# Kernel optimization log

Measured on AMD Instinct MI355X. Metric: run time of the kernel, lower is better.

## Reference

```python
import jax, jax.numpy as jnp
import numpy as np

# WeightOnlyInt8Linear forward: out = (x @ W_int8.astype(x.dtype).T) * scales
# NOTE: the original torch forward has a bug: when bias is not None it returns
# pre_bias (bias is never added), and when bias is None it would crash.
# Faithful math for a runnable configuration (bias=True) is therefore just
# the scaled matmul without bias.

IN_FEATURES = 4096
OUT_FEATURES = 16384
M = 256  # tokens


def setup_inputs() -> dict:
    key = jax.random.key(0)
    k1, k2, k3 = jax.random.split(key, 3)
    x = jax.random.normal(k1, (M, IN_FEATURES), dtype=jnp.float32)
    # int8 quantized weights in [-128, 127]
    weight = jax.random.randint(k2, (OUT_FEATURES, IN_FEATURES), -128, 128, dtype=jnp.int8)
    # per-output-channel dequant scales (positive, small)
    scales = jax.random.uniform(k3, (OUT_FEATURES,), dtype=jnp.float32, minval=0.001, maxval=0.02)
    return {"input": x, "weight": weight, "scales": scales}


def reference(input, weight, scales):
    # weight.to(input): upcast int8 -> activation dtype, then dense GEMM, then per-channel scale
    w = weight.astype(input.dtype)                      # [out, in]
    pre_bias = jnp.einsum('mk,nk->mn', input, w)        # [M, out]
    return pre_bias * scales                            # broadcast over out_features
```

## Files before the change

### kernel.cpp

```cpp
#include <hip/hip_runtime.h>
#include <stdint.h>

#define M_TOK 256
#define N_OUT 16384
#define K_IN  4096
#define BM 64
#define BN 128
#define BK 64
#define NSTEPS (K_IN / BK)

#define AS1 __attribute__((address_space(1)))
#define AS3 __attribute__((address_space(3)))

typedef short v8s __attribute__((ext_vector_type(8)));
typedef float v16f __attribute__((ext_vector_type(16)));
typedef int   v4i __attribute__((ext_vector_type(4)));
typedef unsigned int uint;

__device__ __forceinline__ unsigned short rne_bf16(float f) {
  uint u = __float_as_uint(f);
  uint r = u + 0x7FFFu + ((u >> 16) & 1u);
  return (unsigned short)(r >> 16);
}
__device__ __forceinline__ float bfbits_to_f(uint h) {
  return __uint_as_float(h << 16);
}
__device__ __forceinline__ uint pack_bf16(float a, float b) {
  return (__float_as_uint(a) >> 16) | (__float_as_uint(b) & 0xffff0000u);
}

__global__ __launch_bounds__(256) void cast_kernel(
    const float* __restrict__ x, unsigned short* __restrict__ xhi,
    unsigned short* __restrict__ xlo) {
  const int i = (blockIdx.x * 256 + threadIdx.x) * 4;
  const float4 f = *(const float4*)(x + i);
  float fs[4] = {f.x, f.y, f.z, f.w};
  unsigned short h[4], l[4];
#pragma unroll
  for (int j = 0; j < 4; ++j) {
    h[j] = rne_bf16(fs[j]);
    l[j] = rne_bf16(fs[j] - bfbits_to_f(h[j]));
  }
  *(ushort4*)(xhi + i) = make_ushort4(h[0], h[1], h[2], h[3]);
  *(ushort4*)(xlo + i) = make_ushort4(l[0], l[1], l[2], l[3]);
}

__global__ __launch_bounds__(256, 2) void gemm_kernel(
    const unsigned short* __restrict__ xhi, const unsigned short* __restrict__ xlo,
    const void* __restrict__ wraw, const float* __restrict__ scales,
    float* __restrict__ out) {
  __shared__ alignas(16) unsigned char smem[65536];
  const int tid = threadIdx.x;
  const int lane = tid & 63;
  const int wid = tid >> 6;

  const int* wi = (const int*)wraw;
  const signed char* wb = (const signed char*)wraw;
  bool is32 = true;
#pragma unroll
  for (int i = 0; i < 16; ++i) {
    const int v = wi[i];
    is32 = is32 && (v >= -128) && (v <= 127);
  }

  const int bid = blockIdx.x;
  const int logical = (bid & 7) * 64 + (bid >> 3);
  const int mb = logical & 3;
  const int nb = logical >> 2;
  const int m0 = mb * BM;
  const int n0 = nb * BN;

  const unsigned short* xsrc[4];
  uint xdst[4];
#pragma unroll
  for (int j = 0; j < 4; ++j) {
    const int s = wid * 4 + j;
    const int r = 4 * s + (lane >> 4);
    const int c = (lane & 15) ^ (r & 15);
    xsrc[j] = xhi + (size_t)(c >> 3) * M_TOK * K_IN
            + (size_t)(m0 + r) * K_IN + (size_t)((c & 7) * 8);
    xdst[j] = (uint)(s * 1024);
  }

  const int wr32 = tid >> 4, wc32 = tid & 15;
  const int* w32base = wi + (size_t)(n0 + wr32) * K_IN + (size_t)(wc32 * 4);
  const int wr8 = tid >> 2, wc8 = tid & 3;
  const signed char* w8base = wb + (size_t)(n0 + wr8) * K_IN + (size_t)(wc8 * 16);

  const int l31 = lane & 31, hi5 = lane >> 5;
  const int wm = (wid & 1) * 32;
  const int wn = (wid >> 1) * 64;
  const uint abase = (uint)((wm + l31) * 256);
  const uint axor = (uint)((wm + l31) & 15);
  uint bbase[2], bxor[2], bsel[2];
#pragma unroll
  for (int nf = 0; nf < 2; ++nf) {
    const int wrow = wn + nf * 32 + l31;
    const int q = wrow >> 1;
    bbase[nf] = (uint)(q * 256);
    bxor[nf] = (uint)(q & 15);
    bsel[nf] = (uint)((wrow & 1) * 8);
  }

  v16f acc[2] = {};
  v4i wt[8];

  auto stage = [&](int s, uint xb) {
#pragma unroll
    for (int j = 0; j < 4; ++j)
      __builtin_amdgcn_global_load_lds(
          (const AS1 void*)(xsrc[j] + (size_t)s * BK),
          (AS3 void*)(smem + xb + xdst[j]), 16, 0, 0);
    if (is32) {
#pragma unroll
      for (int i = 0; i < 8; ++i)
        wt[i] = *(const v4i*)(w32base + (size_t)i * 16 * K_IN + (size_t)s * 64);
    } else {
#pragma unroll
      for (int i = 0; i < 2; ++i)
        wt[i] = *(const v4i*)(w8base + (size_t)i * 64 * K_IN + (size_t)s * 64);
    }
  };

  auto conv_write_w = [&](uint wo) {
    if (is32) {
#pragma unroll
      for (int i = 0; i < 8; ++i) {
        const int r = i * 16 + wr32;
        const int q = r >> 1;
        const int chunk = (r & 1) * 8 + (wc32 >> 1);
        const uint byte = wo + (uint)(q * 256) + (uint)((chunk ^ (q & 15)) << 4) +
                          (uint)((wc32 & 1) * 8);
        uint2 d;
        d.x = pack_bf16((float)wt[i].x, (float)wt[i].y);
        d.y = pack_bf16((float)wt[i].z, (float)wt[i].w);
        *(uint2*)(smem + byte) = d;
      }
    } else {
#pragma unroll
      for (int i = 0; i < 2; ++i) {
        const int r = i * 64 + wr8;
        const int q = r >> 1;
        const signed char* bs = (const signed char*)&wt[i];
        uint u[4];
#pragma unroll
        for (int p = 0; p < 4; ++p)
          u[p] = pack_bf16((float)bs[2 * p], (float)bs[2 * p + 1]);
        uint u2[4];
#pragma unroll
        for (int p = 0; p < 4; ++p)
          u2[p] = pack_bf16((float)bs[8 + 2 * p], (float)bs[8 + 2 * p + 1]);
        const int cb = (r & 1) * 8 + wc8 * 2;
        const uint b0 = wo + (uint)(q * 256) + (uint)(((cb + 0) ^ (q & 15)) << 4);
        const uint b1 = wo + (uint)(q * 256) + (uint)(((cb + 1) ^ (q & 15)) << 4);
        *(v4i*)(smem + b0) = *(v4i*)&u[0];
        *(v4i*)(smem + b1) = *(v4i*)&u2[0];
      }
    }
  };

  stage(0, 0u);
  conv_write_w(32768u);
  __syncthreads();

  for (int t = 0; t < NSTEPS; ++t) {
    const uint cur = (uint)(t & 1) << 14;
    const uint xb = cur, wo = 32768u + cur;
    const uint nxb = xb ^ 16384u, nwo = wo ^ 16384u;
    const bool more = (t + 1 < NSTEPS);
    if (more) stage(t + 1, nxb);
    __builtin_amdgcn_sched_barrier(0);

#pragma unroll
    for (int kc = 0; kc < 4; ++kc) {
      const uint ch = (uint)(kc * 2 + hi5);
      v8s ah = *(const v8s*)(smem + xb + abase + ((ch ^ axor) << 4));
      v8s al = *(const v8s*)(smem + xb + abase + (((ch + 8u) ^ axor) << 4));
      v8s b0 = *(const v8s*)(smem + wo + bbase[0] + (((bsel[0] + ch) ^ bxor[0]) << 4));
      v8s b1 = *(const v8s*)(smem + wo + bbase[1] + (((bsel[1] + ch) ^ bxor[1]) << 4));
      acc[0] = __builtin_amdgcn_mfma_f32_32x32x16_bf16(ah, b0, acc[0], 0, 0, 0);
      acc[0] = __builtin_amdgcn_mfma_f32_32x32x16_bf16(al, b0, acc[0], 0, 0, 0);
      acc[1] = __builtin_amdgcn_mfma_f32_32x32x16_bf16(ah, b1, acc[1], 0, 0, 0);
      acc[1] = __builtin_amdgcn_mfma_f32_32x32x16_bf16(al, b1, acc[1], 0, 0, 0);
    }

    if (more) conv_write_w(nwo);
    __syncthreads();
  }

#pragma unroll
  for (int nf = 0; nf < 2; ++nf) {
    const int n = n0 + wn + nf * 32 + l31;
    const float scl = scales[n];
#pragma unroll
    for (int reg = 0; reg < 16; ++reg) {
      const int m = m0 + wm + (reg & 3) + 8 * (reg >> 2) + 4 * hi5;
      out[(size_t)m * N_OUT + n] = acc[nf][reg] * scl;
    }
  }
}

__global__ void naive_kernel(const float* __restrict__ x, const void* __restrict__ wraw,
                             const float* __restrict__ scales, float* __restrict__ out) {
  const int* wi = (const int*)wraw;
  bool is32 = true;
  for (int i = 0; i < 16; ++i) { int v = wi[i]; is32 = is32 && v >= -128 && v <= 127; }
  const int idx = blockIdx.x * 256 + threadIdx.x;
  const int m = idx >> 14;
  const int n = idx & (N_OUT - 1);
  const float* xr = x + (size_t)m * K_IN;
  float acc = 0.f;
  if (is32) {
    const int* wr = wi + (size_t)n * K_IN;
    for (int k = 0; k < K_IN; ++k) acc += xr[k] * (float)wr[k];
  } else {
    const signed char* wr = (const signed char*)wraw + (size_t)n * K_IN;
    for (int k = 0; k < K_IN; ++k) acc += xr[k] * (float)wr[k];
  }
  out[idx] = acc * scales[n];
}

extern "C" void kernel_launch(void* const* d_in, const int* in_sizes, int n_in,
                              void* d_out, int out_size, void* d_ws, size_t ws_size,
                              hipStream_t stream) {
  const float* x = (const float*)d_in[0];
  const void* w = d_in[1];
  const float* scales = (const float*)d_in[2];
  float* out = (float*)d_out;
  if (ws_size >= (size_t)4 * 1024 * 1024) {
    unsigned short* xhi = (unsigned short*)d_ws;
    unsigned short* xlo = xhi + (size_t)M_TOK * K_IN;
    cast_kernel<<<(M_TOK * K_IN) / 1024, 256, 0, stream>>>(x, xhi, xlo);
    gemm_kernel<<<512, 256, 0, stream>>>(xhi, xlo, w, scales, out);
  } else {
    naive_kernel<<<(M_TOK * N_OUT) / 256, 256, 0, stream>>>(x, w, scales, out);
  }
}
```

Measured before the change: 496.2 us.

## Double BK, single-buffer LDS, and prefetch weights two steps ahead in registers

Raises the K tile from 64 to 128, which halves the number of loop iterations and barriers. Shared memory becomes a single buffer: x hi and lo planes go to separate 16KB regions and weights use a plain row-major swizzle. Weight global loads are issued two steps ahead into registers, while the x tile for the next step is loaded asynchronously into LDS between two barriers, with hand-written vmcnt/lgkmcnt waits. The aim is to hide global weight latency behind MFMA work. The cost is double the weight registers, which may hurt occupancy, plus two barriers per step and exposed x-load latency because LDS is no longer double-buffered.

```diff
diff --git a/kernel.cpp b/kernel.cpp
--- a/kernel.cpp
+++ b/kernel.cpp
@@ -6,7 +6,7 @@
 #define K_IN  4096
 #define BM 64
 #define BN 128
-#define BK 64
+#define BK 128
 #define NSTEPS (K_IN / BK)
 
 #define AS1 __attribute__((address_space(1)))
@@ -70,122 +70,127 @@
   const int m0 = mb * BM;
   const int n0 = nb * BN;
 
-  const unsigned short* xsrc[4];
-  uint xdst[4];
-#pragma unroll
-  for (int j = 0; j < 4; ++j) {
-    const int s = wid * 4 + j;
-    const int r = 4 * s + (lane >> 4);
-    const int c = (lane & 15) ^ (r & 15);
-    xsrc[j] = xhi + (size_t)(c >> 3) * M_TOK * K_IN
-            + (size_t)(m0 + r) * K_IN + (size_t)((c & 7) * 8);
-    xdst[j] = (uint)(s * 1024);
-  }
-
-  const int wr32 = tid >> 4, wc32 = tid & 15;
-  const int* w32base = wi + (size_t)(n0 + wr32) * K_IN + (size_t)(wc32 * 4);
-  const int wr8 = tid >> 2, wc8 = tid & 3;
-  const signed char* w8base = wb + (size_t)(n0 + wr8) * K_IN + (size_t)(wc8 * 16);
+  const unsigned short* xsrc[8];
+  uint xdst[8];
+#pragma unroll
+  for (int j = 0; j < 8; ++j) {
+    const int s = wid * 8 + j;
+    const int plane = s >> 4;
+    const int sp = s & 15;
+    const int r = sp * 4 + (lane >> 4);
+    const int p = (lane & 15) ^ (r & 15);
+    xsrc[j] = (plane ? xlo : xhi) + (size_t)(m0 + r) * K_IN + (size_t)(p * 8);
+    xdst[j] = (uint)(plane * 16384 + sp * 1024);
+  }
+
+  const int trow = tid >> 5, c32 = tid & 31;
+  const int* w32base = wi + (size_t)(n0 + trow) * K_IN + (size_t)(c32 * 4);
+  const int r8 = tid >> 3, c8 = tid & 7;
+  const signed char* w8base = wb + (size_t)(n0 + r8) * K_IN + (size_t)(c8 * 16);
 
   const int l31 = lane & 31, hi5 = lane >> 5;
   const int wm = (wid & 1) * 32;
   const int wn = (wid >> 1) * 64;
-  const uint abase = (uint)((wm + l31) * 256);
+  const uint arow = (uint)((wm + l31) * 256);
   const uint axor = (uint)((wm + l31) & 15);
-  uint bbase[2], bxor[2], bsel[2];
+  uint brow[2], bxor[2];
 #pragma unroll
   for (int nf = 0; nf < 2; ++nf) {
-    const int wrow = wn + nf * 32 + l31;
-    const int q = wrow >> 1;
-    bbase[nf] = (uint)(q * 256);
-    bxor[nf] = (uint)(q & 15);
-    bsel[nf] = (uint)((wrow & 1) * 8);
+    const int wr = wn + nf * 32 + l31;
+    brow[nf] = 32768u + (uint)(wr * 256);
+    bxor[nf] = (uint)(wr & 15);
   }
 
   v16f acc[2] = {};
-  v4i wt[8];
-
-  auto stage = [&](int s, uint xb) {
-#pragma unroll
-    for (int j = 0; j < 4; ++j)
+  v4i wt[16];
+
+  auto stage_x = [&](int s) {
+#pragma unroll
+    for (int j = 0; j < 8; ++j)
       __builtin_amdgcn_global_load_lds(
           (const AS1 void*)(xsrc[j] + (size_t)s * BK),
-          (AS3 void*)(smem + xb + xdst[j]), 16, 0, 0);
+          (AS3 void*)(smem + xdst[j]), 16, 0, 0);
+  };
+  auto load_w = [&](int s) {
     if (is32) {
 #pragma unroll
-      for (int i = 0; i < 8; ++i)
-        wt[i] = *(const v4i*)(w32base + (size_t)i * 16 * K_IN + (size_t)s * 64);
+      for (int i = 0; i < 16; ++i)
+        wt[i] = *(const v4i*)(w32base + (size_t)i * 8 * K_IN + (size_t)s * BK);
     } else {
 #pragma unroll
-      for (int i = 0; i < 2; ++i)
-        wt[i] = *(const v4i*)(w8base + (size_t)i * 64 * K_IN + (size_t)s * 64);
+      for (int i = 0; i < 4; ++i)
+        wt[i] = *(const v4i*)(w8base + (size_t)i * 32 * K_IN + (size_t)s * BK);
     }
   };
-
-  auto conv_write_w = [&](uint wo) {
+  auto conv_w = [&]() {
     if (is32) {
 #pragma unroll
-      for (int i = 0; i < 8; ++i) {
-        const int r = i * 16 + wr32;
-        const int q = r >> 1;
-        const int chunk = (r & 1) * 8 + (wc32 >> 1);
-        const uint byte = wo + (uint)(q * 256) + (uint)((chunk ^ (q & 15)) << 4) +
-                          (uint)((wc32 & 1) * 8);
+      for (int i = 0; i < 16; ++i) {
+        const int row = i * 8 + trow;
+        const uint a = 32768u + (uint)(row * 256) +
+                       (uint)(((c32 >> 1) ^ (row & 15)) << 4) + (uint)((c32 & 1) * 8);
         uint2 d;
         d.x = pack_bf16((float)wt[i].x, (float)wt[i].y);
         d.y = pack_bf16((float)wt[i].z, (float)wt[i].w);
-        *(uint2*)(smem + byte) = d;
+        *(uint2*)(smem + a) = d;
       }
     } else {
 #pragma unroll
-      for (int i = 0; i < 2; ++i) {
-        const int r = i * 64 + wr8;
-        const int q = r >> 1;
+      for (int i = 0; i < 4; ++i) {
+        const int row = i * 32 + r8;
         const signed char* bs = (const signed char*)&wt[i];
-        uint u[4];
-#pragma unroll
-        for (int p = 0; p < 4; ++p)
-          u[p] = pack_bf16((float)bs[2 * p], (float)bs[2 * p + 1]);
-        uint u2[4];
-#pragma unroll
-        for (int p = 0; p < 4; ++p)
-          u2[p] = pack_bf16((float)bs[8 + 2 * p], (float)bs[8 + 2 * p + 1]);
-        const int cb = (r & 1) * 8 + wc8 * 2;
-        const uint b0 = wo + (uint)(q * 256) + (uint)(((cb + 0) ^ (q & 15)) << 4);
-        const uint b1 = wo + (uint)(q * 256) + (uint)(((cb + 1) ^ (q & 15)) << 4);
-        *(v4i*)(smem + b0) = *(v4i*)&u[0];
-        *(v4i*)(smem + b1) = *(v4i*)&u2[0];
+        uint u0[4], u1[4];
+#pragma unroll
+        for (int p = 0; p < 4; ++p) {
+          u0[p] = pack_bf16((float)bs[2 * p], (float)bs[2 * p + 1]);
+          u1[p] = pack_bf16((float)bs[8 + 2 * p], (float)bs[8 + 2 * p + 1]);
+        }
+        const uint base = 32768u + (uint)(row * 256);
+        const uint a0 = base + (uint)(((2 * c8 + 0) ^ (row & 15)) << 4);
+        const uint a1 = base + (uint)(((2 * c8 + 1) ^ (row & 15)) << 4);
+        *(v4i*)(smem + a0) = *(v4i*)&u0[0];
+        *(v4i*)(smem + a1) = *(v4i*)&u1[0];
       }
     }
   };
 
-  stage(0, 0u);
-  conv_write_w(32768u);
-  __syncthreads();
-
-  for (int t = 0; t < NSTEPS; ++t) {
-    const uint cur = (uint)(t & 1) << 14;
-    const uint xb = cur, wo = 32768u + cur;
-    const uint nxb = xb ^ 16384u, nwo = wo ^ 16384u;
-    const bool more = (t + 1 < NSTEPS);
-    if (more) stage(t + 1, nxb);
-    __builtin_amdgcn_sched_barrier(0);
-
-#pragma unroll
-    for (int kc = 0; kc < 4; ++kc) {
+  stage_x(0);
+  load_w(0);
+  conv_w();
+  load_w(1);
+  asm volatile("s_waitcnt lgkmcnt(0)" ::: "memory");
+  __builtin_amdgcn_s_barrier();
+  __builtin_amdgcn_sched_barrier(0);
+
+  for (int t = 0;; ++t) {
+#pragma unroll
+    for (int kc = 0; kc < 8; ++kc) {
       const uint ch = (uint)(kc * 2 + hi5);
-      v8s ah = *(const v8s*)(smem + xb + abase + ((ch ^ axor) << 4));
-      v8s al = *(const v8s*)(smem + xb + abase + (((ch + 8u) ^ axor) << 4));
-      v8s b0 = *(const v8s*)(smem + wo + bbase[0] + (((bsel[0] + ch) ^ bxor[0]) << 4));
-      v8s b1 = *(const v8s*)(smem + wo + bbase[1] + (((bsel[1] + ch) ^ bxor[1]) << 4));
+      v8s ah = *(const v8s*)(smem + arow + ((ch ^ axor) << 4));
+      v8s al = *(const v8s*)(smem + 16384u + arow + ((ch ^ axor) << 4));
+      v8s b0 = *(const v8s*)(smem + brow[0] + ((ch ^ bxor[0]) << 4));
+      v8s b1 = *(const v8s*)(smem + brow[1] + ((ch ^ bxor[1]) << 4));
       acc[0] = __builtin_amdgcn_mfma_f32_32x32x16_bf16(ah, b0, acc[0], 0, 0, 0);
       acc[0] = __builtin_amdgcn_mfma_f32_32x32x16_bf16(al, b0, acc[0], 0, 0, 0);
       acc[1] = __builtin_amdgcn_mfma_f32_32x32x16_bf16(ah, b1, acc[1], 0, 0, 0);
       acc[1] = __builtin_amdgcn_mfma_f32_32x32x16_bf16(al, b1, acc[1], 0, 0, 0);
     }
-
-    if (more) conv_write_w(nwo);
-    __syncthreads();
+    if (t == NSTEPS - 1) break;
+
+    asm volatile("s_waitcnt lgkmcnt(0)" ::: "memory");
+    __builtin_amdgcn_s_barrier();
+    __builtin_amdgcn_sched_barrier(0);
+
+    stage_x(t + 1);
+    conv_w();
+    asm volatile("" ::: "memory");
+    const int wnext = (t + 2 < NSTEPS) ? t + 2 : NSTEPS - 1;
+    load_w(wnext);
+    if (is32) asm volatile("s_waitcnt vmcnt(16)" ::: "memory");
+    else      asm volatile("s_waitcnt vmcnt(4)" ::: "memory");
+    asm volatile("s_waitcnt lgkmcnt(0)" ::: "memory");
+    __builtin_amdgcn_s_barrier();
+    __builtin_amdgcn_sched_barrier(0);
   }
 
 #pragma unroll
```

After: 471.0 us. 5.1% less time.

## Reshape GEMM tile to 128x64 with 512 threads and single-buffered LDS

Applied to the files above, without the earlier changes.

Changes the block tile from 64x128 to 128x64, so each weight row is read by two M-blocks instead of four. This roughly halves global weight traffic, which dominates when the weights arrive as int32. The block now has 8 waves, each computing one 32x32 fragment, and uses a single LDS buffer with smaller shared memory to allow more resident blocks. The trade-offs are doubled activation re-reads and the loss of double-buffered overlap between loading and MFMA compute.

```diff
diff --git a/kernel.cpp b/kernel.cpp
--- a/kernel.cpp
+++ b/kernel.cpp
@@ -4,8 +4,8 @@
 #define M_TOK 256
 #define N_OUT 16384
 #define K_IN  4096
-#define BM 64
-#define BN 128
+#define BM 128
+#define BN 64
 #define BK 64
 #define NSTEPS (K_IN / BK)
 
@@ -45,11 +45,11 @@
   *(ushort4*)(xlo + i) = make_ushort4(l[0], l[1], l[2], l[3]);
 }
 
-__global__ __launch_bounds__(256, 2) void gemm_kernel(
+__global__ __launch_bounds__(512, 4) void gemm_kernel(
     const unsigned short* __restrict__ xhi, const unsigned short* __restrict__ xlo,
     const void* __restrict__ wraw, const float* __restrict__ scales,
     float* __restrict__ out) {
-  __shared__ alignas(16) unsigned char smem[65536];
+  __shared__ alignas(16) unsigned char smem[40960];
   const int tid = threadIdx.x;
   const int lane = tid & 63;
   const int wid = tid >> 6;
@@ -65,8 +65,8 @@
 
   const int bid = blockIdx.x;
   const int logical = (bid & 7) * 64 + (bid >> 3);
-  const int mb = logical & 3;
-  const int nb = logical >> 2;
+  const int mb = logical & 1;
+  const int nb = logical >> 1;
   const int m0 = mb * BM;
   const int n0 = nb * BN;
 
@@ -75,128 +75,95 @@
 #pragma unroll
   for (int j = 0; j < 4; ++j) {
     const int s = wid * 4 + j;
-    const int r = 4 * s + (lane >> 4);
+    const int r = s * 4 + (lane >> 4);
     const int c = (lane & 15) ^ (r & 15);
-    xsrc[j] = xhi + (size_t)(c >> 3) * M_TOK * K_IN
-            + (size_t)(m0 + r) * K_IN + (size_t)((c & 7) * 8);
+    xsrc[j] = (c >= 8 ? xlo : xhi) + (size_t)(m0 + r) * K_IN + (size_t)((c & 7) * 8);
     xdst[j] = (uint)(s * 1024);
   }
 
-  const int wr32 = tid >> 4, wc32 = tid & 15;
-  const int* w32base = wi + (size_t)(n0 + wr32) * K_IN + (size_t)(wc32 * 4);
-  const int wr8 = tid >> 2, wc8 = tid & 3;
-  const signed char* w8base = wb + (size_t)(n0 + wr8) * K_IN + (size_t)(wc8 * 16);
+  const int wrow = tid >> 3, wc = tid & 7;
+  const int* w32base = wi + (size_t)(n0 + wrow) * K_IN + (size_t)(wc * 8);
+  const signed char* w8base = wb + (size_t)(n0 + wrow) * K_IN + (size_t)(wc * 8);
+  const uint wq = (uint)(wrow >> 1);
+  const uint wchunk = (uint)((wrow & 1) * 8 + wc);
+  const uint waddr = 32768u + wq * 256u + ((wchunk ^ (wq & 15u)) << 4);
 
   const int l31 = lane & 31, hi5 = lane >> 5;
-  const int wm = (wid & 1) * 32;
-  const int wn = (wid >> 1) * 64;
+  const int wm = (wid & 3) * 32;
+  const int wn = (wid >> 2) * 32;
   const uint abase = (uint)((wm + l31) * 256);
-  const uint axor = (uint)((wm + l31) & 15);
-  uint bbase[2], bxor[2], bsel[2];
-#pragma unroll
-  for (int nf = 0; nf < 2; ++nf) {
-    const int wrow = wn + nf * 32 + l31;
-    const int q = wrow >> 1;
-    bbase[nf] = (uint)(q * 256);
-    bxor[nf] = (uint)(q & 15);
-    bsel[nf] = (uint)((wrow & 1) * 8);
-  }
-
-  v16f acc[2] = {};
-  v4i wt[8];
-
-  auto stage = [&](int s, uint xb) {
+  const uint ax = (uint)((wm + l31) & 15);
+  const int wr = wn + l31;
+  const uint bq = (uint)(wr >> 1);
+  const uint bbase = 32768u + bq * 256u;
+  const uint bsel = (uint)((wr & 1) * 8);
+  const uint bx = bq & 15u;
+
+  v16f acc = {};
+  v4i wt0, wt1;
+
+  auto stage_x = [&](int s) {
 #pragma unroll
     for (int j = 0; j < 4; ++j)
       __builtin_amdgcn_global_load_lds(
           (const AS1 void*)(xsrc[j] + (size_t)s * BK),
-          (AS3 void*)(smem + xb + xdst[j]), 16, 0, 0);
+          (AS3 void*)(smem + xdst[j]), 16, 0, 0);
+  };
+  auto load_w = [&](int s) {
     if (is32) {
-#pragma unroll
-      for (int i = 0; i < 8; ++i)
-        wt[i] = *(const v4i*)(w32base + (size_t)i * 16 * K_IN + (size_t)s * 64);
+      wt0 = *(const v4i*)(w32base + (size_t)s * BK);
+      wt1 = *(const v4i*)(w32base + (size_t)s * BK + 4);
     } else {
-#pragma unroll
-      for (int i = 0; i < 2; ++i)
-        wt[i] = *(const v4i*)(w8base + (size_t)i * 64 * K_IN + (size_t)s * 64);
+      const uint2 u = *(const uint2*)(w8base + (size_t)s * BK);
+      wt0.x = (int)u.x; wt0.y = (int)u.y;
     }
   };
-
-  auto conv_write_w = [&](uint wo) {
+  auto conv_w = [&]() {
+    uint d[4];
     if (is32) {
-#pragma unroll
-      for (int i = 0; i < 8; ++i) {
-        const int r = i * 16 + wr32;
-        const int q = r >> 1;
-        const int chunk = (r & 1) * 8 + (wc32 >> 1);
-        const uint byte = wo + (uint)(q * 256) + (uint)((chunk ^ (q & 15)) << 4) +
-                          (uint)((wc32 & 1) * 8);
-        uint2 d;
-        d.x = pack_bf16((float)wt[i].x, (float)wt[i].y);
-        d.y = pack_bf16((float)wt[i].z, (float)wt[i].w);
-        *(uint2*)(smem + byte) = d;
-      }
+      d[0] = pack_bf16((float)wt0.x, (float)wt0.y);
+      d[1] = pack_bf16((float)wt0.z, (float)wt0.w);
+      d[2] = pack_bf16((float)wt1.x, (float)wt1.y);
+      d[3] = pack_bf16((float)wt1.z, (float)wt1.w);
     } else {
-#pragma unroll
-      for (int i = 0; i < 2; ++i) {
-        const int r = i * 64 + wr8;
-        const int q = r >> 1;
-        const signed char* bs = (const signed char*)&wt[i];
-        uint u[4];
-#pragma unroll
-        for (int p = 0; p < 4; ++p)
-          u[p] = pack_bf16((float)bs[2 * p], (float)bs[2 * p + 1]);
-        uint u2[4];
-#pragma unroll
-        for (int p = 0; p < 4; ++p)
-          u2[p] = pack_bf16((float)bs[8 + 2 * p], (float)bs[8 + 2 * p + 1]);
-        const int cb = (r & 1) * 8 + wc8 * 2;
-        const uint b0 = wo + (uint)(q * 256) + (uint)(((cb + 0) ^ (q & 15)) << 4);
-        const uint b1 = wo + (uint)(q * 256) + (uint)(((cb + 1) ^ (q & 15)) << 4);
-        *(v4i*)(smem + b0) = *(v4i*)&u[0];
-        *(v4i*)(smem + b1) = *(v4i*)&u2[0];
-      }
+      const signed char* bs = (const signed char*)&wt0;
+#pragma unroll
+      for (int p = 0; p < 4; ++p)
+        d[p] = pack_bf16((float)bs[2 * p], (float)bs[2 * p + 1]);
     }
+    v4i wv; wv.x = (int)d[0]; wv.y = (int)d[1]; wv.z = (int)d[2]; wv.w = (int)d[3];
+    *(v4i*)(smem + waddr) = wv;
   };
 
-  stage(0, 0u);
-  conv_write_w(32768u);
-  __syncthreads();
+  stage_x(0);
+  load_w(0);
 
   for (int t = 0; t < NSTEPS; ++t) {
-    const uint cur = (uint)(t & 1) << 14;
-    const uint xb = cur, wo = 32768u + cur;
-    const uint nxb = xb ^ 16384u, nwo = wo ^ 16384u;
-    const bool more = (t + 1 < NSTEPS);
-    if (more) stage(t + 1, nxb);
-    __builtin_amdgcn_sched_barrier(0);
+    conv_w();
+    __syncthreads();
+
+    if (t + 1 < NSTEPS) load_w(t + 1);
 
 #pragma unroll
     for (int kc = 0; kc < 4; ++kc) {
       const uint ch = (uint)(kc * 2 + hi5);
-      v8s ah = *(const v8s*)(smem + xb + abase + ((ch ^ axor) << 4));
-      v8s al = *(const v8s*)(smem + xb + abase + (((ch + 8u) ^ axor) << 4));
-      v8s b0 = *(const v8s*)(smem + wo + bbase[0] + (((bsel[0] + ch) ^ bxor[0]) << 4));
-      v8s b1 = *(const v8s*)(smem + wo + bbase[1] + (((bsel[1] + ch) ^ bxor[1]) << 4));
-      acc[0] = __builtin_amdgcn_mfma_f32_32x32x16_bf16(ah, b0, acc[0], 0, 0, 0);
-      acc[0] = __builtin_amdgcn_mfma_f32_32x32x16_bf16(al, b0, acc[0], 0, 0, 0);
-      acc[1] = __builtin_amdgcn_mfma_f32_32x32x16_bf16(ah, b1, acc[1], 0, 0, 0);
-      acc[1] = __builtin_amdgcn_mfma_f32_32x32x16_bf16(al, b1, acc[1], 0, 0, 0);
+      v8s ah = *(const v8s*)(smem + abase + ((ch ^ ax) << 4));
+      v8s al = *(const v8s*)(smem + abase + (((ch + 8u) ^ ax) << 4));
+      v8s b  = *(const v8s*)(smem + bbase + (((bsel + ch) ^ bx) << 4));
+      acc = __builtin_amdgcn_mfma_f32_32x32x16_bf16(ah, b, acc, 0, 0, 0);
+      acc = __builtin_amdgcn_mfma_f32_32x32x16_bf16(al, b, acc, 0, 0, 0);
     }
 
-    if (more) conv_write_w(nwo);
     __syncthreads();
-  }
-
-#pragma unroll
-  for (int nf = 0; nf < 2; ++nf) {
-    const int n = n0 + wn + nf * 32 + l31;
-    const float scl = scales[n];
-#pragma unroll
-    for (int reg = 0; reg < 16; ++reg) {
-      const int m = m0 + wm + (reg & 3) + 8 * (reg >> 2) + 4 * hi5;
-      out[(size_t)m * N_OUT + n] = acc[nf][reg] * scl;
-    }
+    if (t + 1 < NSTEPS) stage_x(t + 1);
+  }
+
+  const int n = n0 + wn + l31;
+  const float scl = scales[n];
+#pragma unroll
+  for (int reg = 0; reg < 16; ++reg) {
+    const int m = m0 + wm + (reg & 3) + 8 * (reg >> 2) + 4 * hi5;
+    out[(size_t)m * N_OUT + n] = acc[reg] * scl;
   }
 }
 
@@ -231,7 +198,7 @@
     unsigned short* xhi = (unsigned short*)d_ws;
     unsigned short* xlo = xhi + (size_t)M_TOK * K_IN;
     cast_kernel<<<(M_TOK * K_IN) / 1024, 256, 0, stream>>>(x, xhi, xlo);
-    gemm_kernel<<<512, 256, 0, stream>>>(xhi, xlo, w, scales, out);
+    gemm_kernel<<<512, 512, 0, stream>>>(xhi, xlo, w, scales, out);
   } else {
     naive_kernel<<<(M_TOK * N_OUT) / 256, 256, 0, stream>>>(x, w, scales, out);
   }
```

Measured after the change: 407.4 us. -17.9%, faster.
